# Optimization experiments

Measured on AMD Instinct MI355X. Metric: run time of the kernel, lower is better.

## Reference

```python
import jax, jax.numpy as jnp
import numpy as np

B, T, C = 4, 2048, 1024
H = 16
D = C // H  # head_size = 64


def setup_inputs() -> dict:
    key = jax.random.key(0)
    ks = jax.random.split(key, 6)
    s = 0.02
    x = jax.random.normal(ks[0], (B, T, C), dtype=jnp.float32)
    # per-head projections (bias=False), stacked over heads: [H, C, D]
    Wq = jax.random.normal(ks[1], (H, C, D), dtype=jnp.float32) * s
    Wk = jax.random.normal(ks[2], (H, C, D), dtype=jnp.float32) * s
    Wv = jax.random.normal(ks[3], (H, C, D), dtype=jnp.float32) * s
    # output projection Linear(H*D, C)
    Wo = jax.random.normal(ks[4], (H * D, C), dtype=jnp.float32) * s
    bo = jax.random.normal(ks[5], (C,), dtype=jnp.float32) * s
    return {"x": x, "Wq": Wq, "Wk": Wk, "Wv": Wv, "Wo": Wo, "bo": bo}


def reference(x, Wq, Wk, Wv, Wo, bo):
    # q,k,v: [B, H, T, D]
    q = jnp.einsum('btc,hcd->bhtd', x, Wq)
    k = jnp.einsum('btc,hcd->bhtd', x, Wk)
    v = jnp.einsum('btc,hcd->bhtd', x, Wv)
    scale = 1.0 / jnp.sqrt(jnp.asarray(D, dtype=x.dtype))
    scores = jnp.einsum('bhtd,bhsd->bhts', q, k) * scale  # [B,H,T,T]
    causal = jnp.tril(jnp.ones((T, T), dtype=bool))
    scores = jnp.where(causal, scores, jnp.asarray(-jnp.inf, dtype=scores.dtype))
    wei = jax.nn.softmax(scores, axis=-1)
    out = jnp.einsum('bhts,bhsd->bhtd', wei, v)  # [B,H,T,D]
    # concat heads along last dim (head order = module list order)
    out = jnp.transpose(out, (0, 2, 1, 3)).reshape(B, T, H * D)
    return out @ Wo + bo
```

## Files before the change

kernel.cpp:

```cpp
#include <hip/hip_runtime.h>
#include <math.h>

typedef __attribute__((ext_vector_type(8))) short short8;
typedef __attribute__((ext_vector_type(4))) short short4v;
typedef __attribute__((ext_vector_type(4))) float floatx4;

#define AS1 __attribute__((address_space(1)))
#define AS3 __attribute__((address_space(3)))

__device__ inline void gload_lds16(const short* g, short* l) {
    __builtin_amdgcn_global_load_lds((const AS1 unsigned int*)g,
                                     (AS3 unsigned int*)l, 16, 0, 0);
}

__device__ inline short f2bf(float f) {
    unsigned u = __builtin_bit_cast(unsigned, f);
    u += 0x7fffu + ((u >> 16) & 1u);
    return (short)(u >> 16);
}

__global__ __launch_bounds__(256) void conv_x(
    const float* __restrict__ x, short* __restrict__ xb)
{
    int i = (blockIdx.x * 256 + threadIdx.x) * 4;
    float4 v = *(const float4*)&x[i];
    short4v o = { f2bf(v.x), f2bf(v.y), f2bf(v.z), f2bf(v.w) };
    *(short4v*)&xb[i] = o;
}

__global__ __launch_bounds__(256) void transpose_w(
    const float* __restrict__ Wq, const float* __restrict__ Wk,
    const float* __restrict__ Wv, const float* __restrict__ Wo,
    short* __restrict__ Wall, short* __restrict__ WoT)
{
    __shared__ short T[64 * 72];
    const int kt = blockIdx.x, y = blockIdx.y;
    const int tid = threadIdx.x;
    const int lr = tid >> 2, lc = (tid & 3) * 16;
    #pragma unroll 1
    for (int m = 0; m < 4; ++m) {
        const float* src;
        float s = 1.f;
        if (m < 3) {
            const float* W = (m == 0) ? Wq : (m == 1) ? Wk : Wv;
            src = W + ((size_t)y << 16) + (size_t)(kt * 64 + lr) * 64 + lc;
            if (m == 0) s = 0.125f * 1.44269504088896f;
        } else {
            src = Wo + (size_t)(kt * 64 + lr) * 1024 + y * 64 + lc;
        }
        short8 t0, t1;
        {
            float4 v0 = *(const float4*)(src + 0);
            float4 v1 = *(const float4*)(src + 4);
            float4 v2 = *(const float4*)(src + 8);
            float4 v3 = *(const float4*)(src + 12);
            t0[0]=f2bf(v0.x*s); t0[1]=f2bf(v0.y*s); t0[2]=f2bf(v0.z*s); t0[3]=f2bf(v0.w*s);
            t0[4]=f2bf(v1.x*s); t0[5]=f2bf(v1.y*s); t0[6]=f2bf(v1.z*s); t0[7]=f2bf(v1.w*s);
            t1[0]=f2bf(v2.x*s); t1[1]=f2bf(v2.y*s); t1[2]=f2bf(v2.z*s); t1[3]=f2bf(v2.w*s);
            t1[4]=f2bf(v3.x*s); t1[5]=f2bf(v3.y*s); t1[6]=f2bf(v3.z*s); t1[7]=f2bf(v3.w*s);
        }
        *(short8*)&T[lr * 72 + lc]     = t0;
        *(short8*)&T[lr * 72 + lc + 8] = t1;
        __syncthreads();
        short8 o0, o1;
        #pragma unroll
        for (int j = 0; j < 8; ++j) o0[j] = T[(lc + j) * 72 + lr];
        #pragma unroll
        for (int j = 0; j < 8; ++j) o1[j] = T[(lc + 8 + j) * 72 + lr];
        short* dst = (m < 3)
            ? Wall + (size_t)(m * 1024 + y * 64 + lr) * 1024 + kt * 64
            : WoT  + (size_t)(y * 64 + lr) * 1024 + kt * 64;
        *(short8*)&dst[lc]     = o0;
        *(short8*)&dst[lc + 8] = o1;
        __syncthreads();
    }
}

__global__ __launch_bounds__(256) void transpose_v(
    const short* __restrict__ Vp, short* __restrict__ Vt_g)
{
    __shared__ short T[64 * 72];
    const int t0 = blockIdx.x * 64;
    const int h = blockIdx.y, b = blockIdx.z;
    const int tid = threadIdx.x;
    const int r = tid >> 3, c = (tid & 7) * 8;
    #pragma unroll
    for (int p = 0; p < 2; ++p) {
        int t = r + 32 * p;
        *(short8*)&T[t * 72 + c] =
            *(const short8*)&Vp[(size_t)(b * 2048 + t0 + t) * 1024 + h * 64 + c];
    }
    __syncthreads();
    const int d = tid >> 2, tc = (tid & 3) * 16;
    size_t obase = ((size_t)(b * 16 + h)) * 64 * 2048 + (size_t)d * 2048 + t0 + tc;
    short8 o0, o1;
    #pragma unroll
    for (int j = 0; j < 8; ++j) o0[j] = T[(tc + j) * 72 + d];
    #pragma unroll
    for (int j = 0; j < 8; ++j) o1[j] = T[(tc + 8 + j) * 72 + d];
    *(short8*)&Vt_g[obase] = o0;
    *(short8*)&Vt_g[obase + 8] = o1;
}

__global__ __launch_bounds__(256) void gemm_bt(
    const short* __restrict__ A, const short* __restrict__ BT,
    short* __restrict__ C, short* __restrict__ Cv, int M, int N, int K)
{
    __shared__ short As[128 * 32];
    __shared__ short Bs[128 * 32];
    const int tid  = threadIdx.x;
    const int wid  = tid >> 6, lane = tid & 63;
    const int quad = lane >> 4, l15 = lane & 15;
    const int m0 = blockIdx.x * 128, n0 = blockIdx.y * 128;
    const int wr = (wid >> 1) * 64, wc = (wid & 1) * 64;

    floatx4 acc[4][4] = {};

    const int srow = wid * 32 + (lane >> 2);
    const int scol = (lane & 3) * 8;

    for (int k0 = 0; k0 < K; k0 += 32) {
        #pragma unroll
        for (int t = 0; t < 2; ++t) {
            gload_lds16(A  + (size_t)(m0 + srow + t * 16) * K + k0 + scol,
                        &As[(wid * 32 + t * 16) * 32]);
            gload_lds16(BT + (size_t)(n0 + srow + t * 16) * K + k0 + scol,
                        &Bs[(wid * 32 + t * 16) * 32]);
        }
        __syncthreads();
        short8 bfr[4];
        #pragma unroll
        for (int j = 0; j < 4; ++j)
            bfr[j] = *(const short8*)&Bs[(wc + j * 16 + l15) * 32 + quad * 8];
        #pragma unroll
        for (int i = 0; i < 4; ++i) {
            short8 afr = *(const short8*)&As[(wr + i * 16 + l15) * 32 + quad * 8];
            #pragma unroll
            for (int j = 0; j < 4; ++j)
                acc[i][j] = __builtin_amdgcn_mfma_f32_16x16x32_bf16(
                    afr, bfr[j], acc[i][j], 0, 0, 0);
        }
        __syncthreads();
    }

    #pragma unroll
    for (int i = 0; i < 4; ++i) {
        int row = m0 + wr + i * 16 + quad * 4;
        #pragma unroll
        for (int j = 0; j < 4; ++j) {
            int col = n0 + wc + j * 16 + l15;
            int plane = col >> 10, c1 = col & 1023;
            short* dst = (plane == 2) ? Cv : C + (size_t)plane * 8192 * 1024;
            #pragma unroll
            for (int r = 0; r < 4; ++r)
                dst[(size_t)(row + r) * 1024 + c1] = f2bf(acc[i][j][r]);
        }
    }
}

__global__ __launch_bounds__(256) void gemm_o(
    const short* __restrict__ A, const short* __restrict__ BT,
    float* __restrict__ Cf, const float* __restrict__ bias, int N, int K)
{
    __shared__ short As[64 * 32];
    __shared__ short Bs[128 * 32];
    const int tid  = threadIdx.x;
    const int wid  = tid >> 6, lane = tid & 63;
    const int quad = lane >> 4, l15 = lane & 15;
    const int m0 = blockIdx.x * 64, n0 = blockIdx.y * 128;
    const int wr = (wid >> 1) * 32, wc = (wid & 1) * 64;

    floatx4 acc[2][4] = {};

    const int arow = tid >> 2, acol = (tid & 3) * 8;
    const int brow = wid * 32 + (lane >> 2), bcol = (lane & 3) * 8;

    for (int k0 = 0; k0 < K; k0 += 32) {
        gload_lds16(A + (size_t)(m0 + arow) * K + k0 + acol, &As[(wid * 16) * 32]);
        #pragma unroll
        for (int t = 0; t < 2; ++t)
            gload_lds16(BT + (size_t)(n0 + brow + t * 16) * K + k0 + bcol,
                        &Bs[(wid * 32 + t * 16) * 32]);
        __syncthreads();
        short8 bfr[4];
        #pragma unroll
        for (int j = 0; j < 4; ++j)
            bfr[j] = *(const short8*)&Bs[(wc + j * 16 + l15) * 32 + quad * 8];
        #pragma unroll
        for (int i = 0; i < 2; ++i) {
            short8 afr = *(const short8*)&As[(wr + i * 16 + l15) * 32 + quad * 8];
            #pragma unroll
            for (int j = 0; j < 4; ++j)
                acc[i][j] = __builtin_amdgcn_mfma_f32_16x16x32_bf16(
                    afr, bfr[j], acc[i][j], 0, 0, 0);
        }
        __syncthreads();
    }

    #pragma unroll
    for (int i = 0; i < 2; ++i) {
        int row = m0 + wr + i * 16 + quad * 4;
        #pragma unroll
        for (int j = 0; j < 4; ++j) {
            int col = n0 + wc + j * 16 + l15;
            float bv = bias[col];
            #pragma unroll
            for (int r = 0; r < 4; ++r)
                Cf[(size_t)(row + r) * N + col] = acc[i][j][r] + bv;
        }
    }
}

__global__ __launch_bounds__(256) void attn_fwd(
    const short* __restrict__ Q, const short* __restrict__ Kg,
    const short* __restrict__ Vt_g, short* __restrict__ O)
{
    __shared__ short Ks[2][64 * 64];
    __shared__ short Vs[2][64 * 64];
    __shared__ short Pb[4 * 32 * 72];
    const int tid  = threadIdx.x;
    const int wid  = tid >> 6, lane = tid & 63;
    const int quad = lane >> 4, l15 = lane & 15;

    const int flat = blockIdx.x;
    const int xr = flat & 7;
    const int qq = flat >> 3;
    const int qt = 15 - (qq >> 3);
    const int hb = xr * 8 + (qq & 7);
    const int h = hb & 15, b = hb >> 4;

    const size_t base  = ((size_t)b * 2048) * 1024 + h * 64;
    const size_t vbase = ((size_t)(b * 16 + h)) * 64 * 2048;
    short* Pw = &Pb[wid * 32 * 72];

    const int srow = tid >> 3;
    const int gcol = ((tid & 7) ^ (srow & 7)) * 8;
    const int lbase0 = (wid * 8) * 64;
    const int lbase1 = (wid * 8 + 32) * 64;
    const int l7 = l15 & 7;

    const short one_bf = (short)0x3F80;
    const short8 bones = { one_bf, one_bf, one_bf, one_bf,
                           one_bf, one_bf, one_bf, one_bf };

    short8 qf[2][2];
    #pragma unroll
    for (int mt = 0; mt < 2; ++mt)
        #pragma unroll
        for (int ks = 0; ks < 2; ++ks)
            qf[mt][ks] = *(const short8*)&Q[base +
                (size_t)(qt * 128 + wid * 32 + mt * 16 + l15) * 1024 + ks * 32 + quad * 8];

    floatx4 oacc[2][4] = {};
    floatx4 lacc[2] = {};
    const int dst = 2 * qt + (wid >> 1);
    const int nst = 2 * qt + 2;

    const short* kptr = Kg + base + (size_t)srow * 1024 + gcol;
    const short* vptr = Vt_g + vbase + (size_t)srow * 2048 + gcol;

    gload_lds16(kptr,               &Ks[0][lbase0]);
    gload_lds16(kptr + 32 * 1024,   &Ks[0][lbase1]);
    gload_lds16(vptr,               &Vs[0][lbase0]);
    gload_lds16(vptr + 32 * 2048,   &Vs[0][lbase1]);
    kptr += 64 * 1024; vptr += 64;
    __syncthreads();

    for (int st = 0; st < nst; ++st) {
        const short* K0 = Ks[st & 1];
        const short* V0 = Vs[st & 1];
        if (st + 1 < nst) {
            short* K1 = Ks[(st + 1) & 1];
            short* V1 = Vs[(st + 1) & 1];
            gload_lds16(kptr,             &K1[lbase0]);
            gload_lds16(kptr + 32 * 1024, &K1[lbase1]);
            gload_lds16(vptr,             &V1[lbase0]);
            gload_lds16(vptr + 32 * 2048, &V1[lbase1]);
            kptr += 64 * 1024; vptr += 64;
        }

        if (st <= dst) {
            floatx4 sf[2][4];
            #pragma unroll
            for (int nt = 0; nt < 4; ++nt) {
                floatx4 z0 = {}, z1 = {};
                #pragma unroll
                for (int ks = 0; ks < 2; ++ks) {
                    short8 bfr = *(const short8*)&K0[(nt * 16 + l15) * 64 +
                                                     (((ks * 4 + quad) ^ l7) * 8)];
                    z0 = __builtin_amdgcn_mfma_f32_16x16x32_bf16(qf[0][ks], bfr, z0, 0, 0, 0);
                    z1 = __builtin_amdgcn_mfma_f32_16x16x32_bf16(qf[1][ks], bfr, z1, 0, 0, 0);
                }
                sf[0][nt] = z0; sf[1][nt] = z1;
            }

            if (st == dst) {
                #pragma unroll
                for (int mt = 0; mt < 2; ++mt)
                    #pragma unroll
                    for (int nt = 0; nt < 4; ++nt)
                        #pragma unroll
                        for (int r = 0; r < 4; ++r) {
                            int qa = qt * 128 + wid * 32 + mt * 16 + quad * 4 + r;
                            int sa = st * 64 + nt * 16 + l15;
                            if (sa > qa) sf[mt][nt][r] = -INFINITY;
                        }
            }

            #pragma unroll
            for (int mt = 0; mt < 2; ++mt)
                #pragma unroll
                for (int nt = 0; nt < 4; ++nt)
                    #pragma unroll
                    for (int r = 0; r < 4; ++r) {
                        float p = __builtin_amdgcn_exp2f(sf[mt][nt][r]);
                        unsigned u = __builtin_bit_cast(unsigned, p);
                        Pw[(mt * 16 + quad * 4 + r) * 72 + ((nt ^ quad) * 16) + l15] =
                            (short)(u >> 16);
                    }

            #pragma unroll
            for (int ks = 0; ks < 2; ++ks) {
                int blk = (ks * 2 + (quad >> 1)) ^ (l15 >> 2);
                short8 af0 = *(const short8*)&Pw[(l15) * 72 + blk * 16 + (quad & 1) * 8];
                short8 af1 = *(const short8*)&Pw[(16 + l15) * 72 + blk * 16 + (quad & 1) * 8];
                lacc[0] = __builtin_amdgcn_mfma_f32_16x16x32_bf16(af0, bones, lacc[0], 0, 0, 0);
                lacc[1] = __builtin_amdgcn_mfma_f32_16x16x32_bf16(af1, bones, lacc[1], 0, 0, 0);
                #pragma unroll
                for (int nt = 0; nt < 4; ++nt) {
                    short8 bfr = *(const short8*)&V0[(nt * 16 + l15) * 64 +
                                                     (((ks * 4 + quad) ^ l7) * 8)];
                    oacc[0][nt] = __builtin_amdgcn_mfma_f32_16x16x32_bf16(af0, bfr, oacc[0][nt], 0, 0, 0);
                    oacc[1][nt] = __builtin_amdgcn_mfma_f32_16x16x32_bf16(af1, bfr, oacc[1][nt], 0, 0, 0);
                }
            }
        }
        __syncthreads();
    }

    #pragma unroll
    for (int mt = 0; mt < 2; ++mt)
        #pragma unroll
        for (int nt = 0; nt < 4; ++nt)
            #pragma unroll
            for (int r = 0; r < 4; ++r) {
                float v = oacc[mt][nt][r] / lacc[mt][r];
                int qa = qt * 128 + wid * 32 + mt * 16 + quad * 4 + r;
                O[base + (size_t)qa * 1024 + nt * 16 + l15] = f2bf(v);
            }
}

extern "C" void kernel_launch(void* const* d_in, const int* in_sizes, int n_in,
                              void* d_out, int out_size, void* d_ws, size_t ws_size,
                              hipStream_t stream) {
    const float* x  = (const float*)d_in[0];
    const float* Wq = (const float*)d_in[1];
    const float* Wk = (const float*)d_in[2];
    const float* Wv = (const float*)d_in[3];
    const float* Wo = (const float*)d_in[4];
    const float* bo = (const float*)d_in[5];
    float* out = (float*)d_out;

    char* ws = (char*)d_ws;
    const size_t MB = 1024 * 1024;
    short* xb   = (short*)(ws + 0 * MB);
    short* Vt_g = (short*)(ws + 0 * MB);
    short* Vr   = (short*)(ws + 16 * MB);
    short* Ao   = (short*)(ws + 16 * MB);
    short* Wall = (short*)(ws + 32 * MB);
    short* WoT  = (short*)(ws + 38 * MB);
    short* Qp   = (short*)d_out;
    short* Kp   = Qp + 8 * 1024 * 1024;

    conv_x<<<8192, 256, 0, stream>>>(x, xb);
    transpose_w<<<dim3(16, 16), 256, 0, stream>>>(Wq, Wk, Wv, Wo, Wall, WoT);

    gemm_bt<<<dim3(64, 24), 256, 0, stream>>>(xb, Wall, Qp, Vr, 8192, 3072, 1024);
    transpose_v<<<dim3(32, 16, 4), 256, 0, stream>>>(Vr, Vt_g);

    attn_fwd<<<1024, 256, 0, stream>>>(Qp, Kp, Vt_g, Ao);

    gemm_o<<<dim3(128, 8), 256, 0, stream>>>(Ao, WoT, out, bo, 1024, 1024);
}
```

Measured before the change: 270.3 us.

## Fuse V transpose into QKV GEMM epilogue and use swizzled K=64 LDS tiles

Removes the separate transpose_v kernel by having the QKV GEMM epilogue write V directly in transposed [b,h,d,t] layout with 4-element vector stores. Both GEMMs now stage 64-wide K tiles in LDS, halving the number of barrier-separated iterations. They also use an XOR swizzle on the 16-byte chunk index to avoid LDS bank conflicts on fragment reads. This trades a doubled LDS footprint for fewer syncs and one fewer launch and round-trip of V through memory. The transposed V writes are strided across rows, which may coalesce poorly, and the workspace buffers are reassigned.

```diff
diff --git a/kernel.cpp b/kernel.cpp
--- a/kernel.cpp
+++ b/kernel.cpp
@@ -76,84 +76,73 @@
     }
 }
 
-__global__ __launch_bounds__(256) void transpose_v(
-    const short* __restrict__ Vp, short* __restrict__ Vt_g)
-{
-    __shared__ short T[64 * 72];
-    const int t0 = blockIdx.x * 64;
-    const int h = blockIdx.y, b = blockIdx.z;
-    const int tid = threadIdx.x;
-    const int r = tid >> 3, c = (tid & 7) * 8;
-    #pragma unroll
-    for (int p = 0; p < 2; ++p) {
-        int t = r + 32 * p;
-        *(short8*)&T[t * 72 + c] =
-            *(const short8*)&Vp[(size_t)(b * 2048 + t0 + t) * 1024 + h * 64 + c];
-    }
-    __syncthreads();
-    const int d = tid >> 2, tc = (tid & 3) * 16;
-    size_t obase = ((size_t)(b * 16 + h)) * 64 * 2048 + (size_t)d * 2048 + t0 + tc;
-    short8 o0, o1;
-    #pragma unroll
-    for (int j = 0; j < 8; ++j) o0[j] = T[(tc + j) * 72 + d];
-    #pragma unroll
-    for (int j = 0; j < 8; ++j) o1[j] = T[(tc + 8 + j) * 72 + d];
-    *(short8*)&Vt_g[obase] = o0;
-    *(short8*)&Vt_g[obase + 8] = o1;
-}
-
 __global__ __launch_bounds__(256) void gemm_bt(
     const short* __restrict__ A, const short* __restrict__ BT,
-    short* __restrict__ C, short* __restrict__ Cv, int M, int N, int K)
-{
-    __shared__ short As[128 * 32];
-    __shared__ short Bs[128 * 32];
+    short* __restrict__ C, short* __restrict__ Vt, int M, int N, int K)
+{
+    __shared__ short As[128 * 64];
+    __shared__ short Bs[128 * 64];
     const int tid  = threadIdx.x;
     const int wid  = tid >> 6, lane = tid & 63;
     const int quad = lane >> 4, l15 = lane & 15;
+    const int l7 = l15 & 7;
     const int m0 = blockIdx.x * 128, n0 = blockIdx.y * 128;
     const int wr = (wid >> 1) * 64, wc = (wid & 1) * 64;
 
     floatx4 acc[4][4] = {};
 
-    const int srow = wid * 32 + (lane >> 2);
-    const int scol = (lane & 3) * 8;
-
-    for (int k0 = 0; k0 < K; k0 += 32) {
-        #pragma unroll
-        for (int t = 0; t < 2; ++t) {
-            gload_lds16(A  + (size_t)(m0 + srow + t * 16) * K + k0 + scol,
-                        &As[(wid * 32 + t * 16) * 32]);
-            gload_lds16(BT + (size_t)(n0 + srow + t * 16) * K + k0 + scol,
-                        &Bs[(wid * 32 + t * 16) * 32]);
-        }
-        __syncthreads();
-        short8 bfr[4];
-        #pragma unroll
-        for (int j = 0; j < 4; ++j)
-            bfr[j] = *(const short8*)&Bs[(wc + j * 16 + l15) * 32 + quad * 8];
-        #pragma unroll
-        for (int i = 0; i < 4; ++i) {
-            short8 afr = *(const short8*)&As[(wr + i * 16 + l15) * 32 + quad * 8];
+    const int srow = tid >> 3;
+    const int gcol = ((tid & 7) ^ (srow & 7)) * 8;
+
+    for (int k0 = 0; k0 < K; k0 += 64) {
+        #pragma unroll
+        for (int t = 0; t < 4; ++t) {
+            gload_lds16(A  + (size_t)(m0 + srow + t * 32) * K + k0 + gcol,
+                        &As[(t * 32 + wid * 8) * 64]);
+            gload_lds16(BT + (size_t)(n0 + srow + t * 32) * K + k0 + gcol,
+                        &Bs[(t * 32 + wid * 8) * 64]);
+        }
+        __syncthreads();
+        #pragma unroll
+        for (int ks = 0; ks < 2; ++ks) {
+            short8 bfr[4];
             #pragma unroll
             for (int j = 0; j < 4; ++j)
-                acc[i][j] = __builtin_amdgcn_mfma_f32_16x16x32_bf16(
-                    afr, bfr[j], acc[i][j], 0, 0, 0);
-        }
-        __syncthreads();
-    }
-
+                bfr[j] = *(const short8*)&Bs[(wc + j * 16 + l15) * 64 +
+                                             (((ks * 4 + quad) ^ l7) * 8)];
+            #pragma unroll
+            for (int i = 0; i < 4; ++i) {
+                short8 afr = *(const short8*)&As[(wr + i * 16 + l15) * 64 +
+                                                 (((ks * 4 + quad) ^ l7) * 8)];
+                #pragma unroll
+                for (int j = 0; j < 4; ++j)
+                    acc[i][j] = __builtin_amdgcn_mfma_f32_16x16x32_bf16(
+                        afr, bfr[j], acc[i][j], 0, 0, 0);
+            }
+        }
+        __syncthreads();
+    }
+
+    const int plane = n0 >> 10;
     #pragma unroll
     for (int i = 0; i < 4; ++i) {
         int row = m0 + wr + i * 16 + quad * 4;
         #pragma unroll
         for (int j = 0; j < 4; ++j) {
             int col = n0 + wc + j * 16 + l15;
-            int plane = col >> 10, c1 = col & 1023;
-            short* dst = (plane == 2) ? Cv : C + (size_t)plane * 8192 * 1024;
-            #pragma unroll
-            for (int r = 0; r < 4; ++r)
-                dst[(size_t)(row + r) * 1024 + c1] = f2bf(acc[i][j][r]);
+            int c1 = col & 1023;
+            if (plane < 2) {
+                short* dst = C + (size_t)plane * 8192 * 1024;
+                #pragma unroll
+                for (int r = 0; r < 4; ++r)
+                    dst[(size_t)(row + r) * 1024 + c1] = f2bf(acc[i][j][r]);
+            } else {
+                int b = row >> 11, t = row & 2047;
+                int hb = b * 16 + (c1 >> 6), d = c1 & 63;
+                short4v o = { f2bf(acc[i][j][0]), f2bf(acc[i][j][1]),
+                              f2bf(acc[i][j][2]), f2bf(acc[i][j][3]) };
+                *(short4v*)&Vt[((size_t)hb * 64 + d) * 2048 + t] = o;
+            }
         }
     }
 }
@@ -162,37 +151,46 @@
     const short* __restrict__ A, const short* __restrict__ BT,
     float* __restrict__ Cf, const float* __restrict__ bias, int N, int K)
 {
-    __shared__ short As[64 * 32];
-    __shared__ short Bs[128 * 32];
+    __shared__ short As[64 * 64];
+    __shared__ short Bs[128 * 64];
     const int tid  = threadIdx.x;
     const int wid  = tid >> 6, lane = tid & 63;
     const int quad = lane >> 4, l15 = lane & 15;
+    const int l7 = l15 & 7;
     const int m0 = blockIdx.x * 64, n0 = blockIdx.y * 128;
     const int wr = (wid >> 1) * 32, wc = (wid & 1) * 64;
 
     floatx4 acc[2][4] = {};
 
-    const int arow = tid >> 2, acol = (tid & 3) * 8;
-    const int brow = wid * 32 + (lane >> 2), bcol = (lane & 3) * 8;
-
-    for (int k0 = 0; k0 < K; k0 += 32) {
-        gload_lds16(A + (size_t)(m0 + arow) * K + k0 + acol, &As[(wid * 16) * 32]);
+    const int srow = tid >> 3;
+    const int gcol = ((tid & 7) ^ (srow & 7)) * 8;
+
+    for (int k0 = 0; k0 < K; k0 += 64) {
         #pragma unroll
         for (int t = 0; t < 2; ++t)
-            gload_lds16(BT + (size_t)(n0 + brow + t * 16) * K + k0 + bcol,
-                        &Bs[(wid * 32 + t * 16) * 32]);
-        __syncthreads();
-        short8 bfr[4];
-        #pragma unroll
-        for (int j = 0; j < 4; ++j)
-            bfr[j] = *(const short8*)&Bs[(wc + j * 16 + l15) * 32 + quad * 8];
-        #pragma unroll
-        for (int i = 0; i < 2; ++i) {
-            short8 afr = *(const short8*)&As[(wr + i * 16 + l15) * 32 + quad * 8];
+            gload_lds16(A + (size_t)(m0 + srow + t * 32) * K + k0 + gcol,
+                        &As[(t * 32 + wid * 8) * 64]);
+        #pragma unroll
+        for (int t = 0; t < 4; ++t)
+            gload_lds16(BT + (size_t)(n0 + srow + t * 32) * K + k0 + gcol,
+                        &Bs[(t * 32 + wid * 8) * 64]);
+        __syncthreads();
+        #pragma unroll
+        for (int ks = 0; ks < 2; ++ks) {
+            short8 bfr[4];
             #pragma unroll
             for (int j = 0; j < 4; ++j)
-                acc[i][j] = __builtin_amdgcn_mfma_f32_16x16x32_bf16(
-                    afr, bfr[j], acc[i][j], 0, 0, 0);
+                bfr[j] = *(const short8*)&Bs[(wc + j * 16 + l15) * 64 +
+                                             (((ks * 4 + quad) ^ l7) * 8)];
+            #pragma unroll
+            for (int i = 0; i < 2; ++i) {
+                short8 afr = *(const short8*)&As[(wr + i * 16 + l15) * 64 +
+                                                 (((ks * 4 + quad) ^ l7) * 8)];
+                #pragma unroll
+                for (int j = 0; j < 4; ++j)
+                    acc[i][j] = __builtin_amdgcn_mfma_f32_16x16x32_bf16(
+                        afr, bfr[j], acc[i][j], 0, 0, 0);
+            }
         }
         __syncthreads();
     }
@@ -364,9 +362,8 @@
     char* ws = (char*)d_ws;
     const size_t MB = 1024 * 1024;
     short* xb   = (short*)(ws + 0 * MB);
-    short* Vt_g = (short*)(ws + 0 * MB);
-    short* Vr   = (short*)(ws + 16 * MB);
-    short* Ao   = (short*)(ws + 16 * MB);
+    short* Ao   = (short*)(ws + 0 * MB);
+    short* Vt_g = (short*)(ws + 16 * MB);
     short* Wall = (short*)(ws + 32 * MB);
     short* WoT  = (short*)(ws + 38 * MB);
     short* Qp   = (short*)d_out;
@@ -375,8 +372,7 @@
     conv_x<<<8192, 256, 0, stream>>>(x, xb);
     transpose_w<<<dim3(16, 16), 256, 0, stream>>>(Wq, Wk, Wv, Wo, Wall, WoT);
 
-    gemm_bt<<<dim3(64, 24), 256, 0, stream>>>(xb, Wall, Qp, Vr, 8192, 3072, 1024);
-    transpose_v<<<dim3(32, 16, 4), 256, 0, stream>>>(Vr, Vt_g);
+    gemm_bt<<<dim3(64, 24), 256, 0, stream>>>(xb, Wall, Qp, Vt_g, 8192, 3072, 1024);
 
     attn_fwd<<<1024, 256, 0, stream>>>(Qp, Kp, Vt_g, Ao);
 
```

After: 254.7 us. 1.06x faster.
